# Optimization experiments

Measured on AMD Instinct MI355X. Metric: run time of the kernel, lower is better.

## Reference

```python
import jax, jax.numpy as jnp
import numpy as np

FILTER_SIZE = 9
WIN_NUMEL = FILTER_SIZE ** 3  # 729
EPS = 1e-06


def _conv3d_valid(x, w):
    # x: [N,1,D,H,W], w: [1,1,k,k,k]; valid padding, stride 1 (matches F.conv3d padding=0)
    return jax.lax.conv_general_dilated(
        x, w, window_strides=(1, 1, 1), padding='VALID',
        dimension_numbers=('NCDHW', 'OIDHW', 'NCDHW'))


def setup_inputs() -> dict:
    key = jax.random.key(0)
    k1, k2 = jax.random.split(key)
    shape = (1, 1, 160, 160, 160)
    I = jax.random.uniform(k1, shape, dtype=jnp.float32)
    J = jax.random.uniform(k2, shape, dtype=jnp.float32)
    filt = jnp.ones((1, 1, FILTER_SIZE, FILTER_SIZE, FILTER_SIZE), dtype=jnp.float32)
    return {'I': I, 'J': J, 'filt': filt}


def reference(I, J, filt):
    I_sum = _conv3d_valid(I, filt)
    J_sum = _conv3d_valid(J, filt)
    I2_sum = _conv3d_valid(I * I, filt)
    J2_sum = _conv3d_valid(J * J, filt)
    IJ_sum = _conv3d_valid(I * J, filt)

    I_mean = I_sum / WIN_NUMEL
    J_mean = J_sum / WIN_NUMEL

    cross = IJ_sum - I_mean * J_sum - J_mean * I_sum + I_mean * J_mean * WIN_NUMEL
    I_var = I2_sum - 2.0 * I_mean * I_sum + (I_mean ** 2) * WIN_NUMEL
    J_var = J2_sum - 2.0 * J_mean * J_sum + (J_mean ** 2) * WIN_NUMEL

    cc = (cross ** 2) / (I_var * J_var + EPS)
    return 1.0 - jnp.mean(cc)
```

## Files before the change

kernel.cpp:

```cpp
#include <hip/hip_runtime.h>

#define NN 160
#define MM 152
#define TOX 8
#define TOY 32
#define TIX 16
#define TIY 40
#define PS  20
#define PCH (TIY*PS)
#define XST 44
#define XCH (TOX*XST)
#define YST 36
#define YCH (TOX*YST)
#define ZC 19
#define PL 27
#define KMAX 29
#define NTX 19
#define NTILE 95
#define NBLK (NTILE*8)
#define INV_WIN (1.0f/729.0f)

#define STEP_BARRIER() asm volatile("s_waitcnt lgkmcnt(0)\n\ts_barrier" ::: "memory")

__device__ __forceinline__ float cc_of(const float* s) {
    float cross = fmaf(-s[0] * s[1], INV_WIN, s[4]);
    float iv    = fmaf(-s[0] * s[0], INV_WIN, s[2]);
    float jv    = fmaf(-s[1] * s[1], INV_WIN, s[3]);
    return (cross * cross) / (iv * jv + 1e-6f);
}

__global__ __launch_bounds__(256, 4) void lncc_fused(
    const float* __restrict__ I, const float* __restrict__ J,
    float* __restrict__ partial)
{
    __shared__ float Pld[2][2 * PCH];
    __shared__ float xsb[2][5 * XCH];
    __shared__ float ysb[2][5 * YCH];
    __shared__ float red[4];

    const int tid  = threadIdx.x;
    const int orig = blockIdx.x;
    const int bid  = (orig & 7) * NTILE + (orig >> 3);
    const int tile = bid % NTILE;
    const int zc   = bid / NTILE;
    const int x0 = (tile % NTX) * TOX;
    const int y0 = (tile / NTX) * TOY;
    const int z0 = zc * ZC;

    const int yl = tid >> 3, xl = tid & 7;
    const bool valid = (y0 + yl < MM);

    const int rowX = tid >> 1;
    const int qX   = tid & 1;

    const int ce = tid - 80;
    const int r0 = ce >> 2,        q0 = ce & 3;
    const int r1 = (ce + 80) >> 2, q1 = (ce + 80) & 3;
    const size_t gb0 = (size_t)min(y0 + r0, NN - 1) * NN + (x0 + q0 * 4);
    const size_t gb1 = (size_t)min(y0 + r1, NN - 1) * NN + (x0 + q1 * 4);

    const int eY  = tid - 176;
    const int cY  = eY >> 4;
    const int xY  = (eY >> 1) & 7;
    const int yhY = eY & 1;

    float4 pI0, pJ0, pI1, pJ1;
    if (tid >= 80 && tid < 160) {
        const size_t zb = (size_t)z0 * (NN * NN);
        pI0 = *(const float4*)(I + zb + gb0);
        pJ0 = *(const float4*)(J + zb + gb0);
        pI1 = *(const float4*)(I + zb + gb1);
        pJ1 = *(const float4*)(J + zb + gb1);
    }

    float ring[9][5];
    float sz[5] = {0.f, 0.f, 0.f, 0.f, 0.f};
    float cc_acc = 0.f;

    for (int kb = 0; kb <= KMAX; kb += 9) {
#pragma unroll
        for (int ki = 0; ki < 9; ++ki) {
            const int k = kb + ki;
            if (k > KMAX) continue;

            if (k <= PL - 1 && tid >= 80 && tid < 160) {
                float* P = &Pld[k & 1][0];
                *(float4*)&P[r0 * PS + q0 * 4]       = pI0;
                *(float4*)&P[PCH + r0 * PS + q0 * 4] = pJ0;
                *(float4*)&P[r1 * PS + q1 * 4]       = pI1;
                *(float4*)&P[PCH + r1 * PS + q1 * 4] = pJ1;
                if (k <= PL - 2) {
                    const size_t zb = (size_t)(z0 + k + 1) * (NN * NN);
                    pI0 = *(const float4*)(I + zb + gb0);
                    pJ0 = *(const float4*)(J + zb + gb0);
                    pI1 = *(const float4*)(I + zb + gb1);
                    pJ1 = *(const float4*)(J + zb + gb1);
                }
            }

            if (k >= 1 && k <= PL && tid < 80) {
                const int b = (k - 1) & 1;
                const float* P = &Pld[b][0];
                const float4* Ir = (const float4*)&P[rowX * PS + qX * 4];
                const float4* Jr = (const float4*)&P[PCH + rowX * PS + qX * 4];
                float4 i0 = Ir[0], i1 = Ir[1], i2 = Ir[2];
                float4 j0 = Jr[0], j1 = Jr[1], j2 = Jr[2];
                float iv[12], jv[12];
                iv[0]=i0.x; iv[1]=i0.y; iv[2]=i0.z; iv[3]=i0.w;
                iv[4]=i1.x; iv[5]=i1.y; iv[6]=i1.z; iv[7]=i1.w;
                iv[8]=i2.x; iv[9]=i2.y; iv[10]=i2.z; iv[11]=i2.w;
                jv[0]=j0.x; jv[1]=j0.y; jv[2]=j0.z; jv[3]=j0.w;
                jv[4]=j1.x; jv[5]=j1.y; jv[6]=j1.z; jv[7]=j1.w;
                jv[8]=j2.x; jv[9]=j2.y; jv[10]=j2.z; jv[11]=j2.w;
#pragma unroll
                for (int c = 0; c < 5; ++c) {
                    float m[12];
#pragma unroll
                    for (int t = 0; t < 12; ++t) {
                        float av = (c & 1) ? jv[t] : iv[t];
                        float bv = (c < 2) ? 1.0f : ((c == 2) ? iv[t] : jv[t]);
                        m[t] = av * bv;
                    }
                    float s = m[0]+m[1]+m[2]+m[3]+m[4]+m[5]+m[6]+m[7]+m[8];
                    float* W = &xsb[b][c * XCH + rowX];
                    W[(qX * 4) * XST] = s;
#pragma unroll
                    for (int t = 1; t < 4; ++t) {
                        s += m[t + 8] - m[t - 1];
                        W[(qX * 4 + t) * XST] = s;
                    }
                }
            }

            if (k >= 2 && k <= PL + 1 && tid >= 176) {
                const int b = (k - 2) & 1;
                const float* xb = &xsb[b][cY * XCH + xY * XST + yhY * 16];
                float4 w0 = ((const float4*)xb)[0], w1 = ((const float4*)xb)[1],
                       w2 = ((const float4*)xb)[2], w3 = ((const float4*)xb)[3],
                       w4 = ((const float4*)xb)[4], w5 = ((const float4*)xb)[5];
                float m[24];
                m[0]=w0.x;  m[1]=w0.y;  m[2]=w0.z;  m[3]=w0.w;
                m[4]=w1.x;  m[5]=w1.y;  m[6]=w1.z;  m[7]=w1.w;
                m[8]=w2.x;  m[9]=w2.y;  m[10]=w2.z; m[11]=w2.w;
                m[12]=w3.x; m[13]=w3.y; m[14]=w3.z; m[15]=w3.w;
                m[16]=w4.x; m[17]=w4.y; m[18]=w4.z; m[19]=w4.w;
                m[20]=w5.x; m[21]=w5.y; m[22]=w5.z; m[23]=w5.w;
                float o[16];
                float s = m[0]+m[1]+m[2]+m[3]+m[4]+m[5]+m[6]+m[7]+m[8];
                o[0] = s;
#pragma unroll
                for (int t = 1; t < 16; ++t) {
                    s += m[t + 8] - m[t - 1];
                    o[t] = s;
                }
                float* yb = &ysb[b][cY * YCH + xY * YST + yhY * 16];
                float4 oa = {o[0],  o[1],  o[2],  o[3]};
                float4 ob = {o[4],  o[5],  o[6],  o[7]};
                float4 oc = {o[8],  o[9],  o[10], o[11]};
                float4 od = {o[12], o[13], o[14], o[15]};
                ((float4*)yb)[0] = oa; ((float4*)yb)[1] = ob;
                ((float4*)yb)[2] = oc; ((float4*)yb)[3] = od;
            }

            if (k >= 3) {
                const int b = (k - 3) & 1;
                const int slot  = (ki + 6) % 9;
                const int slot2 = (ki + 7) % 9;
                float v[5];
#pragma unroll
                for (int c = 0; c < 5; ++c) {
                    v[c] = ysb[b][c * YCH + xl * YST + yl];
                    sz[c] += v[c];
                    ring[slot][c] = v[c];
                }
                if (k >= 11) {
                    cc_acc += valid ? cc_of(sz) : 0.f;
#pragma unroll
                    for (int c = 0; c < 5; ++c) sz[c] -= ring[slot2][c];
                }
            }

            STEP_BARRIER();
        }
    }

    for (int off = 32; off > 0; off >>= 1)
        cc_acc += __shfl_down(cc_acc, off, 64);
    if ((tid & 63) == 0) red[tid >> 6] = cc_acc;
    __syncthreads();
    if (tid == 0) partial[orig] = red[0] + red[1] + red[2] + red[3];
}

__global__ __launch_bounds__(256) void lncc_final(
    const float* __restrict__ partial, float* __restrict__ out)
{
    double s = 0.0;
    for (int i = threadIdx.x; i < NBLK; i += 256)
        s += (double)partial[i];
    for (int off = 32; off > 0; off >>= 1)
        s += __shfl_down(s, off, 64);
    __shared__ double red[4];
    const int lane = threadIdx.x & 63, wid = threadIdx.x >> 6;
    if (lane == 0) red[wid] = s;
    __syncthreads();
    if (threadIdx.x == 0) {
        double tot = red[0] + red[1] + red[2] + red[3];
        out[0] = (float)(1.0 - tot / ((double)MM * MM * MM));
    }
}

extern "C" void kernel_launch(void* const* d_in, const int* in_sizes, int n_in,
                              void* d_out, int out_size, void* d_ws, size_t ws_size,
                              hipStream_t stream) {
    const float* I = (const float*)d_in[0];
    const float* J = (const float*)d_in[1];

    float* partial = (float*)d_ws;

    lncc_fused<<<NBLK, 256, 0, stream>>>(I, J, partial);
    lncc_final<<<1,    256, 0, stream>>>(partial, (float*)d_out);
    (void)in_sizes; (void)n_in; (void)out_size; (void)ws_size;
}
```

Before: 34.91 us.

## Fuse final reduction via last-block atomic counter and tweak x-pass LDS writes

Removes the separate single-block final reduction kernel: each block writes its partial, bumps a global atomic counter, and the last block to finish does the double-precision sum and writes the output. A memset of the counter is added to the stream in place of the second kernel launch. The x-pass producer warps also get raised scheduling priority, and their four strided LDS stores are merged into two inline-asm ds_write2_b32 instructions. This trades one kernel launch for a memset, a threadfence and an atomic, and the inline asm relies on the address cast and offsets being correct.

```diff
diff --git a/kernel.cpp b/kernel.cpp
--- a/kernel.cpp
+++ b/kernel.cpp
@@ -31,12 +31,15 @@
 
 __global__ __launch_bounds__(256, 4) void lncc_fused(
     const float* __restrict__ I, const float* __restrict__ J,
-    float* __restrict__ partial)
+    float* __restrict__ partial, unsigned* __restrict__ cnt,
+    float* __restrict__ out)
 {
     __shared__ float Pld[2][2 * PCH];
     __shared__ float xsb[2][5 * XCH];
     __shared__ float ysb[2][5 * YCH];
     __shared__ float red[4];
+    __shared__ unsigned lastflag;
+    __shared__ double dred[4];
 
     const int tid  = threadIdx.x;
     const int orig = blockIdx.x;
@@ -99,6 +102,7 @@
             }
 
             if (k >= 1 && k <= PL && tid < 80) {
+                __builtin_amdgcn_s_setprio(1);
                 const int b = (k - 1) & 1;
                 const float* P = &Pld[b][0];
                 const float4* Ir = (const float4*)&P[rowX * PS + qX * 4];
@@ -121,15 +125,19 @@
                         float bv = (c < 2) ? 1.0f : ((c == 2) ? iv[t] : jv[t]);
                         m[t] = av * bv;
                     }
-                    float s = m[0]+m[1]+m[2]+m[3]+m[4]+m[5]+m[6]+m[7]+m[8];
-                    float* W = &xsb[b][c * XCH + rowX];
-                    W[(qX * 4) * XST] = s;
-#pragma unroll
-                    for (int t = 1; t < 4; ++t) {
-                        s += m[t + 8] - m[t - 1];
-                        W[(qX * 4 + t) * XST] = s;
-                    }
-                }
+                    float s0 = m[0]+m[1]+m[2]+m[3]+m[4]+m[5]+m[6]+m[7]+m[8];
+                    float s1 = s0 + m[9]  - m[0];
+                    float s2 = s1 + m[10] - m[1];
+                    float s3 = s2 + m[11] - m[2];
+                    float* W = &xsb[b][c * XCH + rowX + (qX * 4) * XST];
+                    unsigned wa = (unsigned)(uintptr_t)W;
+                    asm volatile(
+                        "ds_write2_b32 %0, %1, %2 offset0:0 offset1:44\n\t"
+                        "ds_write2_b32 %0, %3, %4 offset0:88 offset1:132"
+                        :: "v"(wa), "v"(s0), "v"(s1), "v"(s2), "v"(s3)
+                        : "memory");
+                }
+                __builtin_amdgcn_s_setprio(0);
             }
 
             if (k >= 2 && k <= PL + 1 && tid >= 176) {
@@ -188,24 +196,26 @@
         cc_acc += __shfl_down(cc_acc, off, 64);
     if ((tid & 63) == 0) red[tid >> 6] = cc_acc;
     __syncthreads();
-    if (tid == 0) partial[orig] = red[0] + red[1] + red[2] + red[3];
-}
-
-__global__ __launch_bounds__(256) void lncc_final(
-    const float* __restrict__ partial, float* __restrict__ out)
-{
-    double s = 0.0;
-    for (int i = threadIdx.x; i < NBLK; i += 256)
-        s += (double)partial[i];
-    for (int off = 32; off > 0; off >>= 1)
-        s += __shfl_down(s, off, 64);
-    __shared__ double red[4];
-    const int lane = threadIdx.x & 63, wid = threadIdx.x >> 6;
-    if (lane == 0) red[wid] = s;
+    if (tid == 0) {
+        partial[orig] = red[0] + red[1] + red[2] + red[3];
+        __threadfence();
+        unsigned old = atomicAdd(cnt, 1u);
+        lastflag = (old == NBLK - 1) ? 1u : 0u;
+    }
     __syncthreads();
-    if (threadIdx.x == 0) {
-        double tot = red[0] + red[1] + red[2] + red[3];
-        out[0] = (float)(1.0 - tot / ((double)MM * MM * MM));
+
+    if (lastflag) {
+        double s = 0.0;
+        for (int i = tid; i < NBLK; i += 256)
+            s += (double)partial[i];
+        for (int off = 32; off > 0; off >>= 1)
+            s += __shfl_down(s, off, 64);
+        if ((tid & 63) == 0) dred[tid >> 6] = s;
+        __syncthreads();
+        if (tid == 0) {
+            double tot = dred[0] + dred[1] + dred[2] + dred[3];
+            out[0] = (float)(1.0 - tot / ((double)MM * MM * MM));
+        }
     }
 }
 
@@ -215,9 +225,10 @@
     const float* I = (const float*)d_in[0];
     const float* J = (const float*)d_in[1];
 
-    float* partial = (float*)d_ws;
-
-    lncc_fused<<<NBLK, 256, 0, stream>>>(I, J, partial);
-    lncc_final<<<1,    256, 0, stream>>>(partial, (float*)d_out);
+    float*    partial = (float*)d_ws;
+    unsigned* cnt     = (unsigned*)(partial + NBLK);
+
+    hipMemsetAsync(cnt, 0, sizeof(unsigned), stream);
+    lncc_fused<<<NBLK, 256, 0, stream>>>(I, J, partial, cnt, (float*)d_out);
     (void)in_sizes; (void)n_in; (void)out_size; (void)ws_size;
 }
```

Result: slower. 56.84 us (+62.8%).

## Switch X/Y partial-sum LDS layout to row-major with float4 stores

Applied to the files above, without the earlier changes.

Changes the shared-memory layout of the x-pass and y-pass intermediate buffers from x-major (transposed) to y-row-major with a 12-float row stride. The x-pass now writes four sliding sums as a single float4, and the y-pass reuses a new thread mapping to process four x columns per float4 across four output rows. The intent is to cut scalar/strided LDS accesses and bank conflicts. Launch bounds occupancy hint drops from 4 to 3 blocks per CU, which may raise register budget but reduce occupancy.

```diff
diff --git a/kernel.cpp b/kernel.cpp
--- a/kernel.cpp
+++ b/kernel.cpp
@@ -4,14 +4,12 @@
 #define MM 152
 #define TOX 8
 #define TOY 32
-#define TIX 16
-#define TIY 40
 #define PS  20
-#define PCH (TIY*PS)
-#define XST 44
-#define XCH (TOX*XST)
-#define YST 36
-#define YCH (TOX*YST)
+#define PCH (40*PS)
+#define XR  12
+#define XCH (40*XR+8)
+#define YR  12
+#define YCH (32*YR+8)
 #define ZC 19
 #define PL 27
 #define KMAX 29
@@ -28,8 +26,14 @@
     float jv    = fmaf(-s[1] * s[1], INV_WIN, s[3]);
     return (cross * cross) / (iv * jv + 1e-6f);
 }
-
-__global__ __launch_bounds__(256, 4) void lncc_fused(
+__device__ __forceinline__ float4 f4add(float4 a, float4 b) {
+    float4 r; r.x=a.x+b.x; r.y=a.y+b.y; r.z=a.z+b.z; r.w=a.w+b.w; return r;
+}
+__device__ __forceinline__ float4 f4sub(float4 a, float4 b) {
+    float4 r; r.x=a.x-b.x; r.y=a.y-b.y; r.z=a.z-b.z; r.w=a.w-b.w; return r;
+}
+
+__global__ __launch_bounds__(256, 3) void lncc_fused(
     const float* __restrict__ I, const float* __restrict__ J,
     float* __restrict__ partial)
 {
@@ -61,8 +65,8 @@
 
     const int eY  = tid - 176;
     const int cY  = eY >> 4;
-    const int xY  = (eY >> 1) & 7;
-    const int yhY = eY & 1;
+    const int xqY = (eY >> 3) & 1;
+    const int yqY = eY & 7;
 
     float4 pI0, pJ0, pI1, pJ1;
     if (tid >= 80 && tid < 160) {
@@ -121,45 +125,31 @@
                         float bv = (c < 2) ? 1.0f : ((c == 2) ? iv[t] : jv[t]);
                         m[t] = av * bv;
                     }
-                    float s = m[0]+m[1]+m[2]+m[3]+m[4]+m[5]+m[6]+m[7]+m[8];
-                    float* W = &xsb[b][c * XCH + rowX];
-                    W[(qX * 4) * XST] = s;
-#pragma unroll
-                    for (int t = 1; t < 4; ++t) {
-                        s += m[t + 8] - m[t - 1];
-                        W[(qX * 4 + t) * XST] = s;
-                    }
+                    float s0 = m[0]+m[1]+m[2]+m[3]+m[4]+m[5]+m[6]+m[7]+m[8];
+                    float s1 = s0 + m[9]  - m[0];
+                    float s2 = s1 + m[10] - m[1];
+                    float s3 = s2 + m[11] - m[2];
+                    float4 o; o.x = s0; o.y = s1; o.z = s2; o.w = s3;
+                    *(float4*)&xsb[b][c * XCH + rowX * XR + qX * 4] = o;
                 }
             }
 
             if (k >= 2 && k <= PL + 1 && tid >= 176) {
                 const int b = (k - 2) & 1;
-                const float* xb = &xsb[b][cY * XCH + xY * XST + yhY * 16];
-                float4 w0 = ((const float4*)xb)[0], w1 = ((const float4*)xb)[1],
-                       w2 = ((const float4*)xb)[2], w3 = ((const float4*)xb)[3],
-                       w4 = ((const float4*)xb)[4], w5 = ((const float4*)xb)[5];
-                float m[24];
-                m[0]=w0.x;  m[1]=w0.y;  m[2]=w0.z;  m[3]=w0.w;
-                m[4]=w1.x;  m[5]=w1.y;  m[6]=w1.z;  m[7]=w1.w;
-                m[8]=w2.x;  m[9]=w2.y;  m[10]=w2.z; m[11]=w2.w;
-                m[12]=w3.x; m[13]=w3.y; m[14]=w3.z; m[15]=w3.w;
-                m[16]=w4.x; m[17]=w4.y; m[18]=w4.z; m[19]=w4.w;
-                m[20]=w5.x; m[21]=w5.y; m[22]=w5.z; m[23]=w5.w;
-                float o[16];
-                float s = m[0]+m[1]+m[2]+m[3]+m[4]+m[5]+m[6]+m[7]+m[8];
-                o[0] = s;
-#pragma unroll
-                for (int t = 1; t < 16; ++t) {
-                    s += m[t + 8] - m[t - 1];
-                    o[t] = s;
-                }
-                float* yb = &ysb[b][cY * YCH + xY * YST + yhY * 16];
-                float4 oa = {o[0],  o[1],  o[2],  o[3]};
-                float4 ob = {o[4],  o[5],  o[6],  o[7]};
-                float4 oc = {o[8],  o[9],  o[10], o[11]};
-                float4 od = {o[12], o[13], o[14], o[15]};
-                ((float4*)yb)[0] = oa; ((float4*)yb)[1] = ob;
-                ((float4*)yb)[2] = oc; ((float4*)yb)[3] = od;
+                const float* xb = &xsb[b][cY * XCH + xqY * 4];
+                float4 w[12];
+#pragma unroll
+                for (int j = 0; j < 12; ++j)
+                    w[j] = *(const float4*)&xb[(yqY * 4 + j) * XR];
+                float4 o = f4add(f4add(f4add(f4add(w[0], w[1]), f4add(w[2], w[3])),
+                                 f4add(f4add(w[4], w[5]), f4add(w[6], w[7]))), w[8]);
+                float* yb = &ysb[b][cY * YCH + xqY * 4];
+                *(float4*)&yb[(yqY * 4) * YR] = o;
+#pragma unroll
+                for (int t = 1; t < 4; ++t) {
+                    o = f4add(o, f4sub(w[t + 8], w[t - 1]));
+                    *(float4*)&yb[(yqY * 4 + t) * YR] = o;
+                }
             }
 
             if (k >= 3) {
@@ -169,7 +159,7 @@
                 float v[5];
 #pragma unroll
                 for (int c = 0; c < 5; ++c) {
-                    v[c] = ysb[b][c * YCH + xl * YST + yl];
+                    v[c] = ysb[b][c * YCH + yl * YR + xl];
                     sz[c] += v[c];
                     ring[slot][c] = v[c];
                 }
```

After: 41.27 us. 1.18x slower.
